# Optimization experiments

Measured on AMD Instinct MI355X. Metric: run time of the kernel, lower is better.

Reference implementation:

```python
import jax, jax.numpy as jnp
import numpy as np


def setup_inputs() -> dict:
    key = jax.random.key(0)
    ks = jax.random.split(key, 5)
    B, C, S = 4, 64, 96          # batch, in_c, square spatial size
    H = 8                        # num_heads
    x = jax.random.normal(ks[0], (B, C, S, S), dtype=jnp.float32)
    # 1x1 conv weights stored as (out_c, in_c) matrices
    w_vkq = jax.random.normal(ks[1], (3 * H * C, C), dtype=jnp.float32) * 0.02
    b_vkq = jax.random.normal(ks[2], (3 * H * C,), dtype=jnp.float32) * 0.02
    w_out = jax.random.normal(ks[3], (C, C * H), dtype=jnp.float32) * 0.02
    b_out = jax.random.normal(ks[4], (C,), dtype=jnp.float32) * 0.02
    return {"x": x, "w_vkq": w_vkq, "b_vkq": b_vkq, "w_out": w_out, "b_out": b_out}


def reference(x, w_vkq, b_vkq, w_out, b_out):
    B, C, Hh, W = x.shape                       # module requires Hh == W
    H = w_vkq.shape[0] // (3 * C)               # num_heads
    # to_vkq: 1x1 conv == per-pixel matmul over channels -> (B, 3HC, Hh, W)
    vqk = jnp.einsum('bcxy,oc->boxy', x, w_vkq) + b_vkq[None, :, None, None]
    # torch .view reinterprets spatial (Hh, W) flat buffer as (W, Hh)
    vqk = vqk.reshape(B, 3, H, C, W, Hh)
    v, q, k = vqk[:, 0], vqk[:, 1], vqk[:, 2]
    # channel-wise attention: contract over the 'y' axis, keep channel dim
    h = jnp.einsum('bhcxy,bhczy->bhcxz', v, k) / (W * Hh)   # (B,H,C,W,W)
    h = jax.nn.softmax(h, axis=-1)
    h = jnp.einsum('bhcxy,bhczy->bhcxz', h, q)              # (B,H,C,W,W)
    # rearrange 'b h c x y -> b (c h) x y'  (c outer, h inner)
    h = h.transpose(0, 2, 1, 3, 4).reshape(B, C * H, W, W)
    # to_out: 1x1 conv back to in_c channels
    return jnp.einsum('bkxy,ok->boxy', h, w_out) + b_out[None, :, None, None]
```

## Files before the change

### kernel.cpp

```cpp
#include <hip/hip_runtime.h>
#include <cstdint>
#include <cstddef>

typedef float f32x4 __attribute__((ext_vector_type(4)));
typedef __bf16 bf16x8 __attribute__((ext_vector_type(8)));
typedef uint32_t u32x4 __attribute__((ext_vector_type(4)));

#define TSS 9216
#define KST 104
#define PST 72
#define WST 72
#define RSTD 68

__device__ __forceinline__ uint16_t f2bf(float x) {
  uint32_t u = __float_as_uint(x);
  return (uint16_t)((u + 0x7fffu + ((u >> 16) & 1u)) >> 16);
}
__device__ __forceinline__ uint32_t pack2bf(float a, float b) {
  return (uint32_t)f2bf(a) | ((uint32_t)f2bf(b) << 16);
}

__global__ __launch_bounds__(256, 4) void proj_kernel(
    const float* __restrict__ x, const float* __restrict__ w_vkq,
    const float* __restrict__ b_vkq, uint16_t* __restrict__ vqk)
{
  __shared__ __align__(16) uint16_t Al[128 * PST];
  __shared__ __align__(16) uint16_t Bt[128 * PST];

  const int t  = threadIdx.x;
  const int blk = blockIdx.x;
  const int mt = blk % 12;
  const int bn = blk / 12;
  const int nt = bn % 72;
  const int b  = bn / 72;
  const int m0 = mt * 128, n0 = nt * 128;

  {
    const float4* src = (const float4*)(w_vkq + (size_t)m0 * 64);
    #pragma unroll
    for (int i = 0; i < 8; ++i) {
      const int idx = t + i * 256;
      const int row = idx >> 4;
      const int c4  = (idx & 15) * 4;
      const float4 v = src[idx];
      *(uint2*)&Al[row * PST + c4] = uint2{pack2bf(v.x, v.y), pack2bf(v.z, v.w)};
    }
  }
  {
    const float* __restrict__ xb = x + (size_t)b * 64 * TSS + n0;
    const int p  = t & 127;
    const int c0 = (t >> 7) * 32;
    float v[32];
    #pragma unroll
    for (int i = 0; i < 32; ++i) v[i] = xb[(size_t)(c0 + i) * TSS + p];
    #pragma unroll
    for (int i4 = 0; i4 < 8; ++i4)
      *(uint2*)&Bt[p * PST + c0 + i4 * 4] =
        uint2{pack2bf(v[i4*4+0], v[i4*4+1]), pack2bf(v[i4*4+2], v[i4*4+3])};
  }
  __syncthreads();

  const int L    = t & 63;
  const int w    = t >> 6;
  const int wp   = (w & 1) * 64;
  const int wo   = (w >> 1) * 64;
  const int lcol = L & 15;
  const int lq   = L >> 4;

  const f32x4 zero4 = {0.f, 0.f, 0.f, 0.f};
  f32x4 acc[4][4];
  #pragma unroll
  for (int i = 0; i < 4; ++i)
    #pragma unroll
    for (int j = 0; j < 4; ++j) acc[i][j] = zero4;

  #pragma unroll
  for (int ks = 0; ks < 2; ++ks) {
    bf16x8 af[4], bfr[4];
    #pragma unroll
    for (int tm = 0; tm < 4; ++tm)
      af[tm] = *(const bf16x8*)&Bt[(wp + tm*16 + lcol) * PST + ks*32 + lq*8];
    #pragma unroll
    for (int tn = 0; tn < 4; ++tn)
      bfr[tn] = *(const bf16x8*)&Al[(wo + tn*16 + lcol) * PST + ks*32 + lq*8];
    #pragma unroll
    for (int tm = 0; tm < 4; ++tm)
      #pragma unroll
      for (int tn = 0; tn < 4; ++tn)
        acc[tm][tn] = __builtin_amdgcn_mfma_f32_16x16x32_bf16(af[tm], bfr[tn], acc[tm][tn], 0, 0, 0);
  }

  float bias[4];
  #pragma unroll
  for (int tn = 0; tn < 4; ++tn)
    bias[tn] = b_vkq[m0 + wo + tn*16 + lcol];

  #pragma unroll
  for (int tn = 0; tn < 4; ++tn) {
    const size_t orow = (size_t)(b*1536 + m0 + wo + tn*16 + lcol) * TSS;
    #pragma unroll
    for (int tm = 0; tm < 4; ++tm) {
      const int p = n0 + wp + tm*16 + lq*4;
      const f32x4 a = acc[tm][tn];
      *(uint2*)(vqk + orow + p) =
        uint2{pack2bf(a[0] + bias[tn], a[1] + bias[tn]),
              pack2bf(a[2] + bias[tn], a[3] + bias[tn])};
    }
  }
}

__global__ __launch_bounds__(384, 5) void attn_kernel(uint16_t* __restrict__ vqk)
{
  __shared__ __align__(16) uint16_t Ks[96 * KST];
  __shared__ __align__(16) uint16_t Qs[96 * KST];

  const int t   = threadIdx.x;
  const int blk = blockIdx.x;
  const int b   = blk >> 9;
  const int hc  = blk & 511;
  const size_t pbase = (size_t)(b * 1536 + hc) * TSS;
  const uint16_t* __restrict__ vplane = vqk + pbase;
  const uint16_t* __restrict__ kplane = vqk + pbase + (size_t)1024 * TSS;
  const uint16_t* __restrict__ qplane = vqk + pbase + (size_t)512  * TSS;

  {
    const uint4* __restrict__ sk = (const uint4*)kplane;
    const uint4* __restrict__ sq = (const uint4*)qplane;
    #pragma unroll
    for (int i = 0; i < 3; ++i) {
      const int g   = t + i * 384;
      const int row = g / 12;
      const int off = (g - row * 12) * 8;
      *(uint4*)&Ks[row * KST + off] = sk[g];
      *(uint4*)&Qs[row * KST + off] = sq[g];
    }
  }

  const int L    = t & 63;
  const int w    = t / 64;
  const int lcol = L & 15;
  const int lq   = L >> 4;
  const int xr   = 16 * w;
  const int xrow = xr + lcol;
  const float C  = 1.44269504088896f / 9216.0f;
  const f32x4 zero4 = {0.f, 0.f, 0.f, 0.f};

  bf16x8 bv[3];
  #pragma unroll
  for (int ks = 0; ks < 3; ++ks)
    bv[ks] = *(const bf16x8*)(vplane + (size_t)xrow * 96 + ks*32 + lq*8);

  __syncthreads();

  f32x4 sa[6];
  #pragma unroll
  for (int i = 0; i < 6; ++i) sa[i] = zero4;
  #pragma unroll
  for (int tz = 0; tz < 6; ++tz)
    #pragma unroll
    for (int ks = 0; ks < 3; ++ks) {
      const bf16x8 ak = *(const bf16x8*)&Ks[(tz*16 + lcol) * KST + ks*32 + lq*8];
      sa[tz] = __builtin_amdgcn_mfma_f32_16x16x32_bf16(ak, bv[ks], sa[tz], 0, 0, 0);
    }

  float s = 0.f;
  #pragma unroll
  for (int tz = 0; tz < 6; ++tz)
    #pragma unroll
    for (int r = 0; r < 4; ++r)
      s += __builtin_exp2f(sa[tz][r] * C);
  s += __shfl_xor(s, 16, 64);
  s += __shfl_xor(s, 32, 64);
  const float inv = 1.0f / s;

  __syncthreads();

  #pragma unroll
  for (int tz = 0; tz < 6; ++tz) {
    const float p0 = __builtin_exp2f(sa[tz][0] * C) * inv;
    const float p1 = __builtin_exp2f(sa[tz][1] * C) * inv;
    const float p2 = __builtin_exp2f(sa[tz][2] * C) * inv;
    const float p3 = __builtin_exp2f(sa[tz][3] * C) * inv;
    *(uint2*)&Ks[xrow * KST + tz*16 + lq*4] = uint2{pack2bf(p0, p1), pack2bf(p2, p3)};
  }

  bf16x8 bp[3];
  #pragma unroll
  for (int ks = 0; ks < 3; ++ks)
    bp[ks] = *(const bf16x8*)&Ks[xrow * KST + ks*32 + lq*8];
  f32x4 oa[6];
  #pragma unroll
  for (int i = 0; i < 6; ++i) oa[i] = zero4;
  #pragma unroll
  for (int tz = 0; tz < 6; ++tz)
    #pragma unroll
    for (int ks = 0; ks < 3; ++ks) {
      const bf16x8 aq = *(const bf16x8*)&Qs[(tz*16 + lcol) * KST + ks*32 + lq*8];
      oa[tz] = __builtin_amdgcn_mfma_f32_16x16x32_bf16(aq, bp[ks], oa[tz], 0, 0, 0);
    }

  uint16_t* __restrict__ dst = vqk + pbase;
  #pragma unroll
  for (int tz = 0; tz < 6; ++tz)
    *(uint2*)(dst + (size_t)xrow * 96 + tz*16 + lq*4) =
      uint2{pack2bf(oa[tz][0], oa[tz][1]), pack2bf(oa[tz][2], oa[tz][3])};
}

__global__ __launch_bounds__(256, 4) void out_proj_kernel(
    const uint16_t* __restrict__ attn, const float* __restrict__ w_out,
    const float* __restrict__ b_out, float* __restrict__ out)
{
  __shared__ __align__(16) uint32_t As2[2][32 * RSTD];
  __shared__ __align__(16) uint16_t Wl[2][64 * WST];

  const int t    = threadIdx.x;
  const int blk  = blockIdx.x;
  const int nt   = blk % 144;
  const int b    = blk / 144;
  const int n0   = nt * 64;
  const int L    = t & 63;
  const int w    = t >> 6;
  const int lcol = L & 15;
  const int lq   = L >> 4;
  const int kp_g = t >> 4;
  const int seg  = t & 15;

  const uint16_t* __restrict__ ab = attn + (size_t)b * 1536 * TSS;

  uint2  pa[2][2];
  float4 pw[4];

  auto load_chunk = [&](int k0) {
    #pragma unroll
    for (int i = 0; i < 2; ++i) {
      const int kp = kp_g + i * 16;
      const int ke = k0 + 2*kp, ko = ke + 1;
      const int pe = ((ke & 7) << 6) | (ke >> 3);
      const int po = ((ko & 7) << 6) | (ko >> 3);
      pa[i][0] = *(const uint2*)(ab + (size_t)pe * TSS + n0 + seg * 4);
      pa[i][1] = *(const uint2*)(ab + (size_t)po * TSS + n0 + seg * 4);
    }
    #pragma unroll
    for (int i = 0; i < 4; ++i) {
      const int idx = t + i * 256;
      pw[i] = *(const float4*)(w_out + (size_t)(idx >> 4) * 512 + k0 + (idx & 15) * 4);
    }
  };

  auto store_chunk = [&](int buf) {
    #pragma unroll
    for (int i = 0; i < 2; ++i) {
      const int kp = kp_g + i * 16;
      const uint2 a = pa[i][0], bb = pa[i][1];
      uint4 d;
      d.x = (a.x & 0xffffu) | (bb.x << 16);
      d.y = (a.x >> 16)     | (bb.x & 0xffff0000u);
      d.z = (a.y & 0xffffu) | (bb.y << 16);
      d.w = (a.y >> 16)     | (bb.y & 0xffff0000u);
      *(uint4*)&As2[buf][kp * RSTD + seg * 4] = d;
    }
    #pragma unroll
    for (int i = 0; i < 4; ++i) {
      const int idx = t + i * 256;
      const float4 v = pw[i];
      *(uint2*)&Wl[buf][(idx >> 4) * WST + (idx & 15) * 4] =
        uint2{pack2bf(v.x, v.y), pack2bf(v.z, v.w)};
    }
  };

  f32x4 acc[4];
  const f32x4 zero4 = {0.f, 0.f, 0.f, 0.f};
  #pragma unroll
  for (int tm = 0; tm < 4; ++tm) acc[tm] = zero4;

  load_chunk(0);

  for (int c = 0; c < 8; ++c) {
    const int buf = c & 1;
    store_chunk(buf);
    if (c < 7) load_chunk((c + 1) * 64);
    __syncthreads();
    #pragma unroll
    for (int ks = 0; ks < 2; ++ks) {
      u32x4 bb;
      #pragma unroll
      for (int jj = 0; jj < 4; ++jj)
        bb[jj] = As2[buf][(ks*16 + lq*4 + jj) * RSTD + w*16 + lcol];
      const bf16x8 bfr = __builtin_bit_cast(bf16x8, bb);
      #pragma unroll
      for (int tm = 0; tm < 4; ++tm) {
        const bf16x8 af = *(const bf16x8*)&Wl[buf][(tm*16 + lcol) * WST + ks*32 + lq*8];
        acc[tm] = __builtin_amdgcn_mfma_f32_16x16x32_bf16(af, bfr, acc[tm], 0, 0, 0);
      }
    }
  }

  const int p = n0 + w*16 + lcol;
  #pragma unroll
  for (int tm = 0; tm < 4; ++tm)
    #pragma unroll
    for (int r = 0; r < 4; ++r) {
      const int o = tm*16 + lq*4 + r;
      out[(size_t)(b * 64 + o) * TSS + p] = acc[tm][r] + b_out[o];
    }
}

extern "C" void kernel_launch(void* const* d_in, const int* in_sizes, int n_in,
                              void* d_out, int out_size, void* d_ws, size_t ws_size,
                              hipStream_t stream) {
  const float* x     = (const float*)d_in[0];
  const float* w_vkq = (const float*)d_in[1];
  const float* b_vkq = (const float*)d_in[2];
  const float* w_out = (const float*)d_in[3];
  const float* b_out = (const float*)d_in[4];
  float* out = (float*)d_out;
  uint16_t* vqk = (uint16_t*)d_ws;

  proj_kernel<<<dim3(3456), dim3(256), 0, stream>>>(x, w_vkq, b_vkq, vqk);
  attn_kernel<<<dim3(2048), dim3(384), 0, stream>>>(vqk);
  out_proj_kernel<<<dim3(576), dim3(256), 0, stream>>>(vqk, w_out, b_out, out);
}
```

Measured before the change: 143.8 us.

## Pre-convert projection weights to bf16 and restructure proj kernel per pixel tile

```diff
diff --git a/kernel.cpp b/kernel.cpp
--- a/kernel.cpp
+++ b/kernel.cpp
@@ -4,108 +4,95 @@
 
 typedef float f32x4 __attribute__((ext_vector_type(4)));
 typedef __bf16 bf16x8 __attribute__((ext_vector_type(8)));
+typedef __bf16 bf16x2 __attribute__((ext_vector_type(2)));
 typedef uint32_t u32x4 __attribute__((ext_vector_type(4)));
 
 #define TSS 9216
 #define KST 104
-#define PST 72
+#define XST 72
 #define WST 72
 #define RSTD 68
 
-__device__ __forceinline__ uint16_t f2bf(float x) {
-  uint32_t u = __float_as_uint(x);
-  return (uint16_t)((u + 0x7fffu + ((u >> 16) & 1u)) >> 16);
-}
 __device__ __forceinline__ uint32_t pack2bf(float a, float b) {
-  return (uint32_t)f2bf(a) | ((uint32_t)f2bf(b) << 16);
-}
-
-__global__ __launch_bounds__(256, 4) void proj_kernel(
-    const float* __restrict__ x, const float* __restrict__ w_vkq,
+  bf16x2 v = { (__bf16)a, (__bf16)b };
+  return __builtin_bit_cast(uint32_t, v);
+}
+
+__global__ __launch_bounds__(256, 8) void wcvt_kernel(
+    const float* __restrict__ w, uint16_t* __restrict__ wbf)
+{
+  const int i = blockIdx.x * 256 + threadIdx.x;
+  const float4 v = ((const float4*)w)[i];
+  ((uint2*)wbf)[i] = uint2{pack2bf(v.x, v.y), pack2bf(v.z, v.w)};
+}
+
+__global__ __launch_bounds__(256, 5) void proj_kernel(
+    const float* __restrict__ x, const uint16_t* __restrict__ wbf,
     const float* __restrict__ b_vkq, uint16_t* __restrict__ vqk)
 {
-  __shared__ __align__(16) uint16_t Al[128 * PST];
-  __shared__ __align__(16) uint16_t Bt[128 * PST];
-
-  const int t  = threadIdx.x;
+  __shared__ __align__(16) uint16_t Bt[32 * XST];
+
+  const int t   = threadIdx.x;
   const int blk = blockIdx.x;
-  const int mt = blk % 12;
-  const int bn = blk / 12;
-  const int nt = bn % 72;
-  const int b  = bn / 72;
-  const int m0 = mt * 128, n0 = nt * 128;
-
-  {
-    const float4* src = (const float4*)(w_vkq + (size_t)m0 * 64);
-    #pragma unroll
-    for (int i = 0; i < 8; ++i) {
-      const int idx = t + i * 256;
-      const int row = idx >> 4;
-      const int c4  = (idx & 15) * 4;
-      const float4 v = src[idx];
-      *(uint2*)&Al[row * PST + c4] = uint2{pack2bf(v.x, v.y), pack2bf(v.z, v.w)};
-    }
-  }
+  const int nt  = blk % 288;
+  const int b   = blk / 288;
+  const int n0  = nt * 32;
+
   {
     const float* __restrict__ xb = x + (size_t)b * 64 * TSS + n0;
-    const int p  = t & 127;
-    const int c0 = (t >> 7) * 32;
-    float v[32];
-    #pragma unroll
-    for (int i = 0; i < 32; ++i) v[i] = xb[(size_t)(c0 + i) * TSS + p];
-    #pragma unroll
-    for (int i4 = 0; i4 < 8; ++i4)
-      *(uint2*)&Bt[p * PST + c0 + i4 * 4] =
-        uint2{pack2bf(v[i4*4+0], v[i4*4+1]), pack2bf(v[i4*4+2], v[i4*4+3])};
+    const int p  = t & 31;
+    const int c0 = (t >> 5) * 8;
+    float v[8];
+    #pragma unroll
+    for (int i = 0; i < 8; ++i) v[i] = xb[(size_t)(c0 + i) * TSS + p];
+    *(uint4*)&Bt[p * XST + c0] =
+      uint4{pack2bf(v[0], v[1]), pack2bf(v[2], v[3]),
+            pack2bf(v[4], v[5]), pack2bf(v[6], v[7])};
   }
   __syncthreads();
 
   const int L    = t & 63;
   const int w    = t >> 6;
-  const int wp   = (w & 1) * 64;
-  const int wo   = (w >> 1) * 64;
   const int lcol = L & 15;
   const int lq   = L >> 4;
 
-  const f32x4 zero4 = {0.f, 0.f, 0.f, 0.f};
-  f32x4 acc[4][4];
-  #pragma unroll
-  for (int i = 0; i < 4; ++i)
-    #pragma unroll
-    for (int j = 0; j < 4; ++j) acc[i][j] = zero4;
-
-  #pragma unroll
-  for (int ks = 0; ks < 2; ++ks) {
-    bf16x8 af[4], bfr[4];
-    #pragma unroll
-    for (int tm = 0; tm < 4; ++tm)
-      af[tm] = *(const bf16x8*)&Bt[(wp + tm*16 + lcol) * PST + ks*32 + lq*8];
-    #pragma unroll
-    for (int tn = 0; tn < 4; ++tn)
-      bfr[tn] = *(const bf16x8*)&Al[(wo + tn*16 + lcol) * PST + ks*32 + lq*8];
-    #pragma unroll
-    for (int tm = 0; tm < 4; ++tm)
+  bf16x8 af[2][2];
+  #pragma unroll
+  for (int tm = 0; tm < 2; ++tm)
+    #pragma unroll
+    for (int ks = 0; ks < 2; ++ks)
+      af[tm][ks] = *(const bf16x8*)&Bt[(tm*16 + lcol) * XST + ks*32 + lq*8];
+
+  const int obase = w * 384;
+  bf16x8 bw[2][2];
+  #pragma unroll
+  for (int ks = 0; ks < 2; ++ks)
+    bw[0][ks] = *(const bf16x8*)(wbf + (size_t)(obase + lcol) * 64 + ks*32 + lq*8);
+
+  for (int ot = 0; ot < 24; ++ot) {
+    const int buf = ot & 1;
+    if (ot < 23) {
+      const int on = obase + (ot + 1) * 16 + lcol;
       #pragma unroll
-      for (int tn = 0; tn < 4; ++tn)
-        acc[tm][tn] = __builtin_amdgcn_mfma_f32_16x16x32_bf16(af[tm], bfr[tn], acc[tm][tn], 0, 0, 0);
-  }
-
-  float bias[4];
-  #pragma unroll
-  for (int tn = 0; tn < 4; ++tn)
-    bias[tn] = b_vkq[m0 + wo + tn*16 + lcol];
-
-  #pragma unroll
-  for (int tn = 0; tn < 4; ++tn) {
-    const size_t orow = (size_t)(b*1536 + m0 + wo + tn*16 + lcol) * TSS;
-    #pragma unroll
-    for (int tm = 0; tm < 4; ++tm) {
-      const int p = n0 + wp + tm*16 + lq*4;
-      const f32x4 a = acc[tm][tn];
-      *(uint2*)(vqk + orow + p) =
-        uint2{pack2bf(a[0] + bias[tn], a[1] + bias[tn]),
-              pack2bf(a[2] + bias[tn], a[3] + bias[tn])};
-    }
+      for (int ks = 0; ks < 2; ++ks)
+        bw[buf ^ 1][ks] = *(const bf16x8*)(wbf + (size_t)on * 64 + ks*32 + lq*8);
+    }
+    const int o = obase + ot * 16 + lcol;
+    const float bias = b_vkq[o];
+    f32x4 acc[2];
+    acc[0] = f32x4{bias, bias, bias, bias};
+    acc[1] = acc[0];
+    #pragma unroll
+    for (int tm = 0; tm < 2; ++tm)
+      #pragma unroll
+      for (int ks = 0; ks < 2; ++ks)
+        acc[tm] = __builtin_amdgcn_mfma_f32_16x16x32_bf16(af[tm][ks], bw[buf][ks], acc[tm], 0, 0, 0);
+
+    uint16_t* __restrict__ dst = vqk + (size_t)(b * 1536 + o) * TSS + n0;
+    #pragma unroll
+    for (int tm = 0; tm < 2; ++tm)
+      *(uint2*)(dst + tm*16 + lq*4) =
+        uint2{pack2bf(acc[tm][0], acc[tm][1]), pack2bf(acc[tm][2], acc[tm][3])};
   }
 }
 
@@ -140,8 +127,7 @@
   const int w    = t / 64;
   const int lcol = L & 15;
   const int lq   = L >> 4;
-  const int xr   = 16 * w;
-  const int xrow = xr + lcol;
+  const int xrow = 16 * w + lcol;
   const float C  = 1.44269504088896f / 9216.0f;
   const f32x4 zero4 = {0.f, 0.f, 0.f, 0.f};
 
@@ -315,8 +301,10 @@
   const float* b_out = (const float*)d_in[4];
   float* out = (float*)d_out;
   uint16_t* vqk = (uint16_t*)d_ws;
-
-  proj_kernel<<<dim3(3456), dim3(256), 0, stream>>>(x, w_vkq, b_vkq, vqk);
+  uint16_t* wbf = vqk + (size_t)4*1536*TSS;
+
+  wcvt_kernel<<<dim3(96), dim3(256), 0, stream>>>(w_vkq, wbf);
+  proj_kernel<<<dim3(1152), dim3(256), 0, stream>>>(x, wbf, b_vkq, vqk);
   attn_kernel<<<dim3(2048), dim3(384), 0, stream>>>(vqk);
   out_proj_kernel<<<dim3(576), dim3(256), 0, stream>>>(vqk, w_out, b_out, out);
 }
```

Result: slower. 149.8 us (+4.1%).
